# Optimization experiments

Hardware: AMD Instinct MI355X
Metric: run time of the kernel (lower is better)

## Reference

```python
import jax, jax.numpy as jnp
import numpy as np

TOP_K = 8


def setup_inputs() -> dict:
    key = jax.random.key(0)
    k1, k2, k3 = jax.random.split(key, 3)
    tokens, hidden, experts = 32768, 2048, 64
    hidden_states = jax.random.normal(k1, (tokens, hidden), dtype=jnp.float32)
    weight = jax.random.normal(k2, (experts, hidden), dtype=jnp.float32) * 0.02
    bias = jax.random.normal(k3, (experts,), dtype=jnp.float32) * 0.02
    return {"hidden_states": hidden_states, "weight": weight, "bias": bias}


def reference(hidden_states, weight, bias):
    # router logits: [tokens, experts]
    logits = jnp.einsum('th,eh->te', hidden_states, weight) + bias
    top_vals, top_idx = jax.lax.top_k(logits, TOP_K)            # [tokens, k]
    top_probs = jax.nn.softmax(top_vals, axis=-1)               # softmax over selected k
    rows = jnp.arange(logits.shape[0])[:, None]                  # [tokens, 1]
    scores = jnp.zeros_like(logits).at[rows, top_idx].set(top_probs)
    return scores, top_idx
```

## Files before the change

### kernel.cpp

```cpp
#include <hip/hip_runtime.h>
#include <math.h>

typedef _Float16 half8 __attribute__((ext_vector_type(8)));
typedef float    f32x4 __attribute__((ext_vector_type(4)));

#define TOKENS  32768
#define HIDDEN  2048
#define EXPERTS 64
#define TOPK    8
#define BKW     64
#define NWIN    (HIDDEN / BKW)
#define LDH     72
#define WBUF    (2 * 64 * LDH)

__global__ void wsplit(const float* __restrict__ W,
                       _Float16* __restrict__ whi, _Float16* __restrict__ wlo) {
    int i = blockIdx.x * 256 + threadIdx.x;
    float w = W[i];
    _Float16 h = (_Float16)w;
    whi[i] = h;
    wlo[i] = (_Float16)(w - (float)h);
}

__global__ __launch_bounds__(256, 1)
void router_hyb(const float* __restrict__ A,
                const _Float16* __restrict__ Wh,
                const _Float16* __restrict__ Wl,
                const float* __restrict__ bias,
                float* __restrict__ out) {
    __shared__ __align__(16) _Float16 hsm[2 * WBUF];
    const int tid = threadIdx.x;
    const int wv  = tid >> 6;
    const int l   = tid & 63;
    const int g   = blockIdx.x;

    const int we = tid >> 2;
    const int wc = tid & 3;
    const _Float16* WhB = Wh + (size_t)we * HIDDEN;
    const _Float16* WlB = Wl + (size_t)we * HIDDEN;

    const float* pa = A + ((size_t)(g * 64 + wv * 16 + (l & 15))) * HIDDEN + (l >> 4) * 8;

    const int ko0 = (l >> 4) * 8;
    const int ko1 = 32 + ko0;

    f32x4 acc[4];
    #pragma unroll
    for (int n = 0; n < 4; ++n) acc[n] = (f32x4){0.f, 0.f, 0.f, 0.f};

    float4 aA0, aA1, aA2, aA3;
    float4 aB0, aB1, aB2, aB3;
    half8 swh0, swh1, swl0, swl1;

    #define LOADA(S, win) do {                                               \
        const float* p_ = pa + (win) * BKW;                                  \
        a##S##0 = *(const float4*)(p_);                                      \
        a##S##1 = *(const float4*)(p_ + 4);                                  \
        a##S##2 = *(const float4*)(p_ + 32);                                 \
        a##S##3 = *(const float4*)(p_ + 36);                                 \
    } while (0)

    #define LOADW(win) do {                                                  \
        swh0 = *(const half8*)(WhB + (win) * BKW + wc * 8);                  \
        swh1 = *(const half8*)(WhB + (win) * BKW + wc * 8 + 32);             \
        swl0 = *(const half8*)(WlB + (win) * BKW + wc * 8);                  \
        swl1 = *(const half8*)(WlB + (win) * BKW + wc * 8 + 32);             \
    } while (0)

    #define STOREW(B) do {                                                   \
        *(half8*)(&hsm[(B) + we * LDH + wc * 8])                = swh0;      \
        *(half8*)(&hsm[(B) + we * LDH + wc * 8 + 32])           = swh1;      \
        *(half8*)(&hsm[(B) + 64 * LDH + we * LDH + wc * 8])      = swl0;     \
        *(half8*)(&hsm[(B) + 64 * LDH + we * LDH + wc * 8 + 32]) = swl1;     \
    } while (0)

    #define CVT8(HI, LO, V0, V1) do {                                        \
        float f_[8] = {(V0).x, (V0).y, (V0).z, (V0).w,                       \
                       (V1).x, (V1).y, (V1).z, (V1).w};                      \
        _Pragma("unroll")                                                    \
        for (int j_ = 0; j_ < 8; ++j_) {                                     \
            _Float16 h_ = (_Float16)f_[j_];                                  \
            (HI)[j_] = h_;                                                   \
            (LO)[j_] = (_Float16)(f_[j_] - (float)h_);                       \
        }                                                                    \
    } while (0)

    #define MFMA_STEP(B, AH, AL, KO) do {                                    \
        _Pragma("unroll")                                                    \
        for (int n = 0; n < 4; ++n) {                                        \
            half8 bh = *(const half8*)(&hsm[(B) + (n * 16 + (l & 15)) * LDH + (KO)]); \
            half8 bl = *(const half8*)(&hsm[(B) + 64 * LDH + (n * 16 + (l & 15)) * LDH + (KO)]); \
            acc[n] = __builtin_amdgcn_mfma_f32_16x16x32_f16(AH, bh, acc[n], 0, 0, 0); \
            acc[n] = __builtin_amdgcn_mfma_f32_16x16x32_f16(AH, bl, acc[n], 0, 0, 0); \
            acc[n] = __builtin_amdgcn_mfma_f32_16x16x32_f16(AL, bh, acc[n], 0, 0, 0); \
        }                                                                    \
    } while (0)

    #define PHASE(B, S, win) do {                                            \
        half8 ahi0, alo0, ahi1, alo1;                                        \
        CVT8(ahi0, alo0, a##S##0, a##S##1);                                  \
        CVT8(ahi1, alo1, a##S##2, a##S##3);                                  \
        if ((win) + 2 < NWIN) LOADA(S, (win) + 2);   \
        MFMA_STEP(B, ahi0, alo0, ko0);                                       \
        MFMA_STEP(B, ahi1, alo1, ko1);                                       \
    } while (0)

    LOADA(A, 0);
    LOADA(B, 1);
    LOADW(0);
    STOREW(0);
    __syncthreads();

    #pragma unroll 1
    for (int s = 0; s < NWIN; s += 2) {
        if (s + 1 < NWIN) LOADW(s + 1);
        PHASE(0, A, s);
        if (s + 1 < NWIN) STOREW(WBUF);
        __syncthreads();

        if (s + 2 < NWIN) LOADW(s + 2);
        PHASE(WBUF, B, s + 1);
        if (s + 2 < NWIN) STOREW(0);
        __syncthreads();
    }
    #undef LOADA
    #undef LOADW
    #undef STOREW
    #undef CVT8
    #undef MFMA_STEP
    #undef PHASE

    float* lg = (float*)hsm;
    float* sc = (float*)hsm + 64 * 68;

    #pragma unroll
    for (int n = 0; n < 4; ++n) {
        float b = bias[n * 16 + (l & 15)];
        #pragma unroll
        for (int q = 0; q < 4; ++q) {
            int trow = wv * 16 + (l >> 4) * 4 + q;
            lg[trow * 68 + n * 16 + (l & 15)] = acc[n][q] + b;
        }
    }
    for (int i = tid; i < 64 * 65; i += 256) sc[i] = 0.f;
    __syncthreads();

    if (tid < 64) {
        const int t = tid;
        float v[64];
        #pragma unroll
        for (int e = 0; e < 64; ++e) v[e] = lg[t * 68 + e];

        float tvals[TOPK]; int tix[TOPK]; float probs[TOPK];
        unsigned long long chosen = 0ull;
        #pragma unroll
        for (int j = 0; j < TOPK; ++j) {
            float best = -INFINITY; int bi = 0;
            #pragma unroll
            for (int e = 0; e < 64; ++e) {
                bool ok = ((chosen >> e) & 1ull) == 0ull;
                if (ok && v[e] > best) { best = v[e]; bi = e; }
            }
            chosen |= (1ull << bi);
            tvals[j] = best; tix[j] = bi;
        }
        float m = tvals[0];
        float ssum = 0.f;
        #pragma unroll
        for (int j = 0; j < TOPK; ++j) { probs[j] = __expf(tvals[j] - m); ssum += probs[j]; }
        float inv = 1.f / ssum;
        #pragma unroll
        for (int j = 0; j < TOPK; ++j) probs[j] *= inv;

        #pragma unroll
        for (int j = 0; j < TOPK; ++j) sc[t * 65 + tix[j]] = probs[j];

        float* oidx = out + (size_t)TOKENS * EXPERTS;
        const int token = g * 64 + t;
        #pragma unroll
        for (int j = 0; j < TOPK; ++j) oidx[(size_t)token * TOPK + j] = (float)tix[j];
    }
    __syncthreads();

    float* oscore = out + (size_t)g * 4096;
    #pragma unroll
    for (int p = 0; p < 4; ++p) {
        int fi  = tid + 256 * p;
        int tok = fi >> 4;
        int es  = (fi & 15) * 4;
        float4 vv;
        vv.x = sc[tok * 65 + es + 0];
        vv.y = sc[tok * 65 + es + 1];
        vv.z = sc[tok * 65 + es + 2];
        vv.w = sc[tok * 65 + es + 3];
        *(float4*)(oscore + (size_t)fi * 4) = vv;
    }
}

extern "C" void kernel_launch(void* const* d_in, const int* in_sizes, int n_in,
                              void* d_out, int out_size, void* d_ws, size_t ws_size,
                              hipStream_t stream) {
    const float* A    = (const float*)d_in[0];
    const float* W    = (const float*)d_in[1];
    const float* bias = (const float*)d_in[2];
    float* out = (float*)d_out;

    _Float16* whi = (_Float16*)d_ws;
    _Float16* wlo = whi + EXPERTS * HIDDEN;

    wsplit<<<512, 256, 0, stream>>>(W, whi, wlo);
    router_hyb<<<TOKENS / 64, 256, 0, stream>>>(A, whi, wlo, bias, out);
}
```

Baseline: 69.21 us.

## Stream pre-swizzled fp16 weight tiles into LDS with direct global-to-LDS loads

The weight split kernel now also packs each 128-wide K window into an XOR-swizzled tile layout. The main kernel copies those tiles straight into LDS with global_load_lds, which removes the register round-trip and the explicit LDS stores. The K window doubles to 128, halving the number of barriers, and the A prefetch now loads one window ahead instead of two. The trade-offs are more live registers for the A prefetch and reliance on the async LDS-load path finishing before each barrier.

Result: slower. 73.07 us (+5.6%).

```diff
diff --git a/kernel.cpp b/kernel.cpp
--- a/kernel.cpp
+++ b/kernel.cpp
@@ -8,70 +8,74 @@
 #define HIDDEN  2048
 #define EXPERTS 64
 #define TOPK    8
-#define BKW     64
+#define BKW     128
 #define NWIN    (HIDDEN / BKW)
-#define LDH     72
-#define WBUF    (2 * 64 * LDH)
-
-__global__ void wsplit(const float* __restrict__ W,
-                       _Float16* __restrict__ whi, _Float16* __restrict__ wlo) {
-    int i = blockIdx.x * 256 + threadIdx.x;
-    float w = W[i];
-    _Float16 h = (_Float16)w;
-    whi[i] = h;
-    wlo[i] = (_Float16)(w - (float)h);
+#define WROW    128
+#define WBUFB   32768
+
+#define GLB(p) ((const __attribute__((address_space(1))) char*)(p))
+#define LDS(p) ((__attribute__((address_space(3))) char*)(p))
+
+__global__ void wsplit_pack(const float* __restrict__ W,
+                            _Float16* __restrict__ whp, _Float16* __restrict__ wlp) {
+    int id = blockIdx.x * 256 + threadIdx.x;
+    int win = id >> 10;
+    int er  = (id >> 4) & 63;
+    int c   = id & 15;
+    int k0  = win * BKW + ((c ^ (er & 7)) << 3);
+    const float* src = W + (size_t)er * HIDDEN + k0;
+    float4 v0 = *(const float4*)(src);
+    float4 v1 = *(const float4*)(src + 4);
+    float f[8] = {v0.x, v0.y, v0.z, v0.w, v1.x, v1.y, v1.z, v1.w};
+    half8 hi, lo;
+    #pragma unroll
+    for (int j = 0; j < 8; ++j) {
+        _Float16 h = (_Float16)f[j];
+        hi[j] = h;
+        lo[j] = (_Float16)(f[j] - (float)h);
+    }
+    *(half8*)(whp + (size_t)id * 8) = hi;
+    *(half8*)(wlp + (size_t)id * 8) = lo;
 }
 
 __global__ __launch_bounds__(256, 1)
-void router_hyb(const float* __restrict__ A,
-                const _Float16* __restrict__ Wh,
-                const _Float16* __restrict__ Wl,
-                const float* __restrict__ bias,
-                float* __restrict__ out) {
-    __shared__ __align__(16) _Float16 hsm[2 * WBUF];
+void router_gl(const float* __restrict__ A,
+               const _Float16* __restrict__ WhP,
+               const _Float16* __restrict__ WlP,
+               const float* __restrict__ bias,
+               float* __restrict__ out) {
+    __shared__ __align__(1024) char smem[2 * WBUFB];
     const int tid = threadIdx.x;
     const int wv  = tid >> 6;
     const int l   = tid & 63;
     const int g   = blockIdx.x;
 
-    const int we = tid >> 2;
-    const int wc = tid & 3;
-    const _Float16* WhB = Wh + (size_t)we * HIDDEN;
-    const _Float16* WlB = Wl + (size_t)we * HIDDEN;
-
-    const float* pa = A + ((size_t)(g * 64 + wv * 16 + (l & 15))) * HIDDEN + (l >> 4) * 8;
-
-    const int ko0 = (l >> 4) * 8;
-    const int ko1 = 32 + ko0;
+    const float* pa = A + ((size_t)(g * 64 + wv * 16 + (l & 15))) * HIDDEN + ((l >> 4) << 3);
 
     f32x4 acc[4];
     #pragma unroll
     for (int n = 0; n < 4; ++n) acc[n] = (f32x4){0.f, 0.f, 0.f, 0.f};
 
-    float4 aA0, aA1, aA2, aA3;
-    float4 aB0, aB1, aB2, aB3;
-    half8 swh0, swh1, swl0, swl1;
+    float4 qA0, qA1, qA2, qA3, qA4, qA5, qA6, qA7;
+    float4 qB0, qB1, qB2, qB3, qB4, qB5, qB6, qB7;
 
     #define LOADA(S, win) do {                                               \
         const float* p_ = pa + (win) * BKW;                                  \
-        a##S##0 = *(const float4*)(p_);                                      \
-        a##S##1 = *(const float4*)(p_ + 4);                                  \
-        a##S##2 = *(const float4*)(p_ + 32);                                 \
-        a##S##3 = *(const float4*)(p_ + 36);                                 \
-    } while (0)
-
-    #define LOADW(win) do {                                                  \
-        swh0 = *(const half8*)(WhB + (win) * BKW + wc * 8);                  \
-        swh1 = *(const half8*)(WhB + (win) * BKW + wc * 8 + 32);             \
-        swl0 = *(const half8*)(WlB + (win) * BKW + wc * 8);                  \
-        swl1 = *(const half8*)(WlB + (win) * BKW + wc * 8 + 32);             \
-    } while (0)
-
-    #define STOREW(B) do {                                                   \
-        *(half8*)(&hsm[(B) + we * LDH + wc * 8])                = swh0;      \
-        *(half8*)(&hsm[(B) + we * LDH + wc * 8 + 32])           = swh1;      \
-        *(half8*)(&hsm[(B) + 64 * LDH + we * LDH + wc * 8])      = swl0;     \
-        *(half8*)(&hsm[(B) + 64 * LDH + we * LDH + wc * 8 + 32]) = swl1;     \
+        q##S##0 = *(const float4*)(p_);        q##S##1 = *(const float4*)(p_ + 4);    \
+        q##S##2 = *(const float4*)(p_ + 32);   q##S##3 = *(const float4*)(p_ + 36);   \
+        q##S##4 = *(const float4*)(p_ + 64);   q##S##5 = *(const float4*)(p_ + 68);   \
+        q##S##6 = *(const float4*)(p_ + 96);   q##S##7 = *(const float4*)(p_ + 100);  \
+    } while (0)
+
+    #define GLOADW(win, bufoff) do {                                         \
+        _Pragma("unroll")                                                    \
+        for (int i_ = 0; i_ < 4; ++i_) {                                     \
+            const size_t go_ = (size_t)(win) * 16384 + (wv * 16 + i_ * 4) * 256 + l * 16; \
+            char* dh_ = smem + (bufoff) + (wv * 16 + i_ * 4) * 256;          \
+            char* dl_ = dh_ + 16384;                                         \
+            __builtin_amdgcn_global_load_lds(GLB((const char*)WhP + go_), LDS(dh_), 16, 0, 0); \
+            __builtin_amdgcn_global_load_lds(GLB((const char*)WlP + go_), LDS(dl_), 16, 0, 0); \
+        }                                                                    \
     } while (0)
 
     #define CVT8(HI, LO, V0, V1) do {                                        \
@@ -85,53 +89,56 @@
         }                                                                    \
     } while (0)
 
-    #define MFMA_STEP(B, AH, AL, KO) do {                                    \
+    #define KTILE(bufoff, KT, V0, V1) do {                                   \
+        half8 ahi_, alo_;                                                    \
+        CVT8(ahi_, alo_, V0, V1);                                            \
+        const _Float16* wh_ = (const _Float16*)(smem + (bufoff));            \
+        const _Float16* wl_ = (const _Float16*)(smem + (bufoff) + 16384);    \
         _Pragma("unroll")                                                    \
         for (int n = 0; n < 4; ++n) {                                        \
-            half8 bh = *(const half8*)(&hsm[(B) + (n * 16 + (l & 15)) * LDH + (KO)]); \
-            half8 bl = *(const half8*)(&hsm[(B) + 64 * LDH + (n * 16 + (l & 15)) * LDH + (KO)]); \
-            acc[n] = __builtin_amdgcn_mfma_f32_16x16x32_f16(AH, bh, acc[n], 0, 0, 0); \
-            acc[n] = __builtin_amdgcn_mfma_f32_16x16x32_f16(AH, bl, acc[n], 0, 0, 0); \
-            acc[n] = __builtin_amdgcn_mfma_f32_16x16x32_f16(AL, bh, acc[n], 0, 0, 0); \
+            const int er_ = n * 16 + (l & 15);                               \
+            const int cp_ = (((KT) * 4 + (l >> 4)) ^ (er_ & 7)) << 3;        \
+            half8 bh = *(const half8*)(wh_ + er_ * WROW + cp_);              \
+            half8 bl = *(const half8*)(wl_ + er_ * WROW + cp_);              \
+            acc[n] = __builtin_amdgcn_mfma_f32_16x16x32_f16(ahi_, bh, acc[n], 0, 0, 0); \
+            acc[n] = __builtin_amdgcn_mfma_f32_16x16x32_f16(ahi_, bl, acc[n], 0, 0, 0); \
+            acc[n] = __builtin_amdgcn_mfma_f32_16x16x32_f16(alo_, bh, acc[n], 0, 0, 0); \
         }                                                                    \
     } while (0)
 
-    #define PHASE(B, S, win) do {                                            \
-        half8 ahi0, alo0, ahi1, alo1;                                        \
-        CVT8(ahi0, alo0, a##S##0, a##S##1);                                  \
-        CVT8(ahi1, alo1, a##S##2, a##S##3);                                  \
-        if ((win) + 2 < NWIN) LOADA(S, (win) + 2);   \
-        MFMA_STEP(B, ahi0, alo0, ko0);                                       \
-        MFMA_STEP(B, ahi1, alo1, ko1);                                       \
-    } while (0)
-
+    #define COMPUTE(bufoff, S) do {                                          \
+        KTILE(bufoff, 0, q##S##0, q##S##1);                                  \
+        KTILE(bufoff, 1, q##S##2, q##S##3);                                  \
+        KTILE(bufoff, 2, q##S##4, q##S##5);                                  \
+        KTILE(bufoff, 3, q##S##6, q##S##7);                                  \
+    } while (0)
+
+    GLOADW(0, 0);
     LOADA(A, 0);
-    LOADA(B, 1);
-    LOADW(0);
-    STOREW(0);
     __syncthreads();
 
     #pragma unroll 1
     for (int s = 0; s < NWIN; s += 2) {
-        if (s + 1 < NWIN) LOADW(s + 1);
-        PHASE(0, A, s);
-        if (s + 1 < NWIN) STOREW(WBUF);
+        GLOADW(s + 1, WBUFB);
+        LOADA(B, s + 1);
+        COMPUTE(0, A);
         __syncthreads();
 
-        if (s + 2 < NWIN) LOADW(s + 2);
-        PHASE(WBUF, B, s + 1);
-        if (s + 2 < NWIN) STOREW(0);
+        if (s + 2 < NWIN) {
+            GLOADW(s + 2, 0);
+            LOADA(A, s + 2);
+        }
+        COMPUTE(WBUFB, B);
         __syncthreads();
     }
     #undef LOADA
-    #undef LOADW
-    #undef STOREW
+    #undef GLOADW
     #undef CVT8
-    #undef MFMA_STEP
-    #undef PHASE
-
-    float* lg = (float*)hsm;
-    float* sc = (float*)hsm + 64 * 68;
+    #undef KTILE
+    #undef COMPUTE
+
+    float* lg = (float*)smem;
+    float* sc = (float*)smem + 64 * 68;
 
     #pragma unroll
     for (int n = 0; n < 4; ++n) {
@@ -205,9 +212,9 @@
     const float* bias = (const float*)d_in[2];
     float* out = (float*)d_out;
 
-    _Float16* whi = (_Float16*)d_ws;
-    _Float16* wlo = whi + EXPERTS * HIDDEN;
-
-    wsplit<<<512, 256, 0, stream>>>(W, whi, wlo);
-    router_hyb<<<TOKENS / 64, 256, 0, stream>>>(A, whi, wlo, bias, out);
+    _Float16* whp = (_Float16*)d_ws;
+    _Float16* wlp = whp + EXPERTS * HIDDEN;
+
+    wsplit_pack<<<64, 256, 0, stream>>>(W, whp, wlp);
+    router_gl<<<TOKENS / 64, 256, 0, stream>>>(A, whp, wlp, bias, out);
 }
```

## Split hidden dimension across wave groups and double token tile per block

Applied to the files above, without the earlier changes.

Blocks now hold 128 tokens with 512 threads; two groups of four waves each compute half of the hidden dimension and combine partial logits through shared memory. Each wave handles two 16-row blocks, so each W fragment loaded from LDS feeds twice as many MFMAs. The aim is more memory parallelism per CU and less LDS traffic per FLOP, at the cost of an extra cross-group reduction, more registers and a single resident block per CU.

Result: slower. 73.24 us (+5.8%).

```diff
diff --git a/kernel.cpp b/kernel.cpp
--- a/kernel.cpp
+++ b/kernel.cpp
@@ -8,10 +8,12 @@
 #define HIDDEN  2048
 #define EXPERTS 64
 #define TOPK    8
+#define TB      128
+#define KHALF   1024
 #define BKW     64
-#define NWIN    (HIDDEN / BKW)
+#define NWIN    (KHALF / BKW)
 #define LDH     72
-#define WBUF    (2 * 64 * LDH)
+#define REGH    (2 * 64 * LDH)
 
 __global__ void wsplit(const float* __restrict__ W,
                        _Float16* __restrict__ whi, _Float16* __restrict__ wlo) {
@@ -22,42 +24,49 @@
     wlo[i] = (_Float16)(w - (float)h);
 }
 
-__global__ __launch_bounds__(256, 1)
-void router_hyb(const float* __restrict__ A,
-                const _Float16* __restrict__ Wh,
-                const _Float16* __restrict__ Wl,
-                const float* __restrict__ bias,
-                float* __restrict__ out) {
-    __shared__ __align__(16) _Float16 hsm[2 * WBUF];
+__global__ __launch_bounds__(512, 1)
+void router_ks(const float* __restrict__ A,
+               const _Float16* __restrict__ Wh,
+               const _Float16* __restrict__ Wl,
+               const float* __restrict__ bias,
+               float* __restrict__ out) {
+    __shared__ __align__(16) _Float16 hsm[4 * REGH];
     const int tid = threadIdx.x;
     const int wv  = tid >> 6;
     const int l   = tid & 63;
     const int g   = blockIdx.x;
-
-    const int we = tid >> 2;
+    const int h   = wv >> 2;
+    const int q   = wv & 3;
+
+    const float* pa = A + ((size_t)(g * TB + q * 32 + (l & 15))) * HIDDEN
+                        + h * KHALF + ((l >> 4) << 3);
+    const float* pb = pa + (size_t)16 * HIDDEN;
+
+    const int er = (tid & 255) >> 2;
     const int wc = tid & 3;
-    const _Float16* WhB = Wh + (size_t)we * HIDDEN;
-    const _Float16* WlB = Wl + (size_t)we * HIDDEN;
-
-    const float* pa = A + ((size_t)(g * 64 + wv * 16 + (l & 15))) * HIDDEN + (l >> 4) * 8;
-
-    const int ko0 = (l >> 4) * 8;
-    const int ko1 = 32 + ko0;
-
-    f32x4 acc[4];
+    const _Float16* WhB = Wh + (size_t)er * HIDDEN + h * KHALF;
+    const _Float16* WlB = Wl + (size_t)er * HIDDEN + h * KHALF;
+
+    _Float16* reg0 = hsm + (h * 2 + 0) * REGH;
+    _Float16* reg1 = hsm + (h * 2 + 1) * REGH;
+
+    f32x4 acc[2][4];
     #pragma unroll
-    for (int n = 0; n < 4; ++n) acc[n] = (f32x4){0.f, 0.f, 0.f, 0.f};
-
-    float4 aA0, aA1, aA2, aA3;
-    float4 aB0, aB1, aB2, aB3;
+    for (int rb = 0; rb < 2; ++rb)
+        #pragma unroll
+        for (int n = 0; n < 4; ++n) acc[rb][n] = (f32x4){0.f, 0.f, 0.f, 0.f};
+
+    float4 qA0, qA1, qA2, qA3, qA4, qA5, qA6, qA7;
+    float4 qB0, qB1, qB2, qB3, qB4, qB5, qB6, qB7;
     half8 swh0, swh1, swl0, swl1;
 
     #define LOADA(S, win) do {                                               \
-        const float* p_ = pa + (win) * BKW;                                  \
-        a##S##0 = *(const float4*)(p_);                                      \
-        a##S##1 = *(const float4*)(p_ + 4);                                  \
-        a##S##2 = *(const float4*)(p_ + 32);                                 \
-        a##S##3 = *(const float4*)(p_ + 36);                                 \
+        const float* pa_ = pa + (win) * BKW;                                 \
+        const float* pb_ = pb + (win) * BKW;                                 \
+        q##S##0 = *(const float4*)(pa_);      q##S##1 = *(const float4*)(pa_ + 4);  \
+        q##S##2 = *(const float4*)(pa_ + 32); q##S##3 = *(const float4*)(pa_ + 36); \
+        q##S##4 = *(const float4*)(pb_);      q##S##5 = *(const float4*)(pb_ + 4);  \
+        q##S##6 = *(const float4*)(pb_ + 32); q##S##7 = *(const float4*)(pb_ + 36); \
     } while (0)
 
     #define LOADW(win) do {                                                  \
@@ -67,11 +76,11 @@
         swl1 = *(const half8*)(WlB + (win) * BKW + wc * 8 + 32);             \
     } while (0)
 
-    #define STOREW(B) do {                                                   \
-        *(half8*)(&hsm[(B) + we * LDH + wc * 8])                = swh0;      \
-        *(half8*)(&hsm[(B) + we * LDH + wc * 8 + 32])           = swh1;      \
-        *(half8*)(&hsm[(B) + 64 * LDH + we * LDH + wc * 8])      = swl0;     \
-        *(half8*)(&hsm[(B) + 64 * LDH + we * LDH + wc * 8 + 32]) = swl1;     \
+    #define STOREW(R) do {                                                   \
+        *(half8*)(&(R)[er * LDH + wc * 8])                 = swh0;           \
+        *(half8*)(&(R)[er * LDH + wc * 8 + 32])            = swh1;           \
+        *(half8*)(&(R)[64 * LDH + er * LDH + wc * 8])      = swl0;           \
+        *(half8*)(&(R)[64 * LDH + er * LDH + wc * 8 + 32]) = swl1;           \
     } while (0)
 
     #define CVT8(HI, LO, V0, V1) do {                                        \
@@ -85,67 +94,86 @@
         }                                                                    \
     } while (0)
 
-    #define MFMA_STEP(B, AH, AL, KO) do {                                    \
+    #define KSLICE(R, RB, KO, V0, V1) do {                                   \
+        half8 ahi_, alo_;                                                    \
+        CVT8(ahi_, alo_, V0, V1);                                            \
         _Pragma("unroll")                                                    \
         for (int n = 0; n < 4; ++n) {                                        \
-            half8 bh = *(const half8*)(&hsm[(B) + (n * 16 + (l & 15)) * LDH + (KO)]); \
-            half8 bl = *(const half8*)(&hsm[(B) + 64 * LDH + (n * 16 + (l & 15)) * LDH + (KO)]); \
-            acc[n] = __builtin_amdgcn_mfma_f32_16x16x32_f16(AH, bh, acc[n], 0, 0, 0); \
-            acc[n] = __builtin_amdgcn_mfma_f32_16x16x32_f16(AH, bl, acc[n], 0, 0, 0); \
-            acc[n] = __builtin_amdgcn_mfma_f32_16x16x32_f16(AL, bh, acc[n], 0, 0, 0); \
+            half8 bh = *(const half8*)(&(R)[(n * 16 + (l & 15)) * LDH + (KO)]); \
+            half8 bl = *(const half8*)(&(R)[64 * LDH + (n * 16 + (l & 15)) * LDH + (KO)]); \
+            acc[RB][n] = __builtin_amdgcn_mfma_f32_16x16x32_f16(ahi_, bh, acc[RB][n], 0, 0, 0); \
+            acc[RB][n] = __builtin_amdgcn_mfma_f32_16x16x32_f16(ahi_, bl, acc[RB][n], 0, 0, 0); \
+            acc[RB][n] = __builtin_amdgcn_mfma_f32_16x16x32_f16(alo_, bh, acc[RB][n], 0, 0, 0); \
         }                                                                    \
     } while (0)
 
-    #define PHASE(B, S, win) do {                                            \
-        half8 ahi0, alo0, ahi1, alo1;                                        \
-        CVT8(ahi0, alo0, a##S##0, a##S##1);                                  \
-        CVT8(ahi1, alo1, a##S##2, a##S##3);                                  \
-        if ((win) + 2 < NWIN) LOADA(S, (win) + 2);   \
-        MFMA_STEP(B, ahi0, alo0, ko0);                                       \
-        MFMA_STEP(B, ahi1, alo1, ko1);                                       \
-    } while (0)
-
+    #define COMPUTE(R, S) do {                                               \
+        const int ko0_ = (l >> 4) << 3;                                      \
+        KSLICE(R, 0, ko0_,      q##S##0, q##S##1);                           \
+        KSLICE(R, 1, ko0_,      q##S##4, q##S##5);                           \
+        KSLICE(R, 0, ko0_ + 32, q##S##2, q##S##3);                           \
+        KSLICE(R, 1, ko0_ + 32, q##S##6, q##S##7);                           \
+    } while (0)
+
+    LOADW(0);
+    STOREW(reg0);
     LOADA(A, 0);
-    LOADA(B, 1);
-    LOADW(0);
-    STOREW(0);
     __syncthreads();
 
     #pragma unroll 1
     for (int s = 0; s < NWIN; s += 2) {
-        if (s + 1 < NWIN) LOADW(s + 1);
-        PHASE(0, A, s);
-        if (s + 1 < NWIN) STOREW(WBUF);
+        LOADW(s + 1);
+        LOADA(B, s + 1);
+        COMPUTE(reg0, A);
+        STOREW(reg1);
         __syncthreads();
 
-        if (s + 2 < NWIN) LOADW(s + 2);
-        PHASE(WBUF, B, s + 1);
-        if (s + 2 < NWIN) STOREW(0);
+        if (s + 2 < NWIN) {
+            LOADW(s + 2);
+            LOADA(A, s + 2);
+        }
+        COMPUTE(reg1, B);
+        if (s + 2 < NWIN) STOREW(reg0);
         __syncthreads();
     }
     #undef LOADA
     #undef LOADW
     #undef STOREW
     #undef CVT8
-    #undef MFMA_STEP
-    #undef PHASE
+    #undef KSLICE
+    #undef COMPUTE
 
     float* lg = (float*)hsm;
-    float* sc = (float*)hsm + 64 * 68;
-
-    #pragma unroll
-    for (int n = 0; n < 4; ++n) {
-        float b = bias[n * 16 + (l & 15)];
-        #pragma unroll
-        for (int q = 0; q < 4; ++q) {
-            int trow = wv * 16 + (l >> 4) * 4 + q;
-            lg[trow * 68 + n * 16 + (l & 15)] = acc[n][q] + b;
-        }
-    }
-    for (int i = tid; i < 64 * 65; i += 256) sc[i] = 0.f;
-    __syncthreads();
-
-    if (tid < 64) {
+    float* sc = (float*)hsm + TB * 68;
+
+    if (h == 1) {
+        #pragma unroll
+        for (int rb = 0; rb < 2; ++rb)
+            #pragma unroll
+            for (int n = 0; n < 4; ++n)
+                #pragma unroll
+                for (int j = 0; j < 4; ++j)
+                    lg[(q * 32 + rb * 16 + (l >> 4) * 4 + j) * 68 + n * 16 + (l & 15)]
+                        = acc[rb][n][j];
+    }
+    __syncthreads();
+    if (h == 0) {
+        #pragma unroll
+        for (int rb = 0; rb < 2; ++rb)
+            #pragma unroll
+            for (int n = 0; n < 4; ++n) {
+                float b = bias[n * 16 + (l & 15)];
+                #pragma unroll
+                for (int j = 0; j < 4; ++j) {
+                    int idx = (q * 32 + rb * 16 + (l >> 4) * 4 + j) * 68 + n * 16 + (l & 15);
+                    lg[idx] = lg[idx] + acc[rb][n][j] + b;
+                }
+            }
+    }
+    for (int i = tid; i < TB * 65; i += 512) sc[i] = 0.f;
+    __syncthreads();
+
+    if (tid < TB) {
         const int t = tid;
         float v[64];
         #pragma unroll
@@ -176,16 +204,16 @@
         for (int j = 0; j < TOPK; ++j) sc[t * 65 + tix[j]] = probs[j];
 
         float* oidx = out + (size_t)TOKENS * EXPERTS;
-        const int token = g * 64 + t;
+        const int token = g * TB + t;
         #pragma unroll
         for (int j = 0; j < TOPK; ++j) oidx[(size_t)token * TOPK + j] = (float)tix[j];
     }
     __syncthreads();
 
-    float* oscore = out + (size_t)g * 4096;
+    float* oscore = out + (size_t)g * (TB * 64);
     #pragma unroll
     for (int p = 0; p < 4; ++p) {
-        int fi  = tid + 256 * p;
+        int fi  = tid + 512 * p;
         int tok = fi >> 4;
         int es  = (fi & 15) * 4;
         float4 vv;
@@ -209,5 +237,5 @@
     _Float16* wlo = whi + EXPERTS * HIDDEN;
 
     wsplit<<<512, 256, 0, stream>>>(W, whi, wlo);
-    router_hyb<<<TOKENS / 64, 256, 0, stream>>>(A, whi, wlo, bias, out);
+    router_ks<<<TOKENS / TB, 512, 0, stream>>>(A, whi, wlo, bias, out);
 }
```
